# Kernel optimization log

Measured on AMD Instinct MI355X. Metric: run time of the kernel, lower is better.

The kernel has to match this reference:

```python
import jax, jax.numpy as jnp
import numpy as np

B, N, D = 64, 4096, 256      # batch, num_inputs, in_features
S, K, H = 11, 128, 256       # num_slots, slot_size, mlp_hidden_size
ITERS = 3
EPS = 1e-6
LN_EPS = 1e-5


def layer_norm(x, w, b):
    m = jnp.mean(x, axis=-1, keepdims=True)
    v = jnp.mean(jnp.square(x - m), axis=-1, keepdims=True)
    return (x - m) * jax.lax.rsqrt(v + LN_EPS) * w + b


def setup_inputs() -> dict:
    key = jax.random.key(0)
    ks = jax.random.split(key, 24)
    rn = lambda i, shape, sc=1.0: jax.random.normal(ks[i], shape, jnp.float32) * sc
    p = 0.05  # param init scale
    return {
        "inputs": rn(0, (B, N, D)),
        "slots_init": rn(1, (B, S, K)),
        "slots_mu": rn(2, (1, 1, K), p),
        "slots_log_sigma": rn(3, (1, 1, K), p),
        "ln_in_w": 1.0 + rn(4, (D,), p), "ln_in_b": rn(5, (D,), p),
        "ln_slot_w": 1.0 + rn(6, (K,), p), "ln_slot_b": rn(7, (K,), p),
        "ln_mlp_w": 1.0 + rn(8, (K,), p), "ln_mlp_b": rn(9, (K,), p),
        "Wq": rn(10, (K, K), p),
        "Wk": rn(11, (K, D), p),
        "Wv": rn(12, (K, D), p),
        "w_ih": rn(13, (3 * K, K), p), "w_hh": rn(14, (3 * K, K), p),
        "b_ih": rn(15, (3 * K,), p), "b_hh": rn(16, (3 * K,), p),
        "mlp_w1": rn(17, (H, K), p), "mlp_b1": rn(18, (H,), p),
        "mlp_w2": rn(19, (K, H), p), "mlp_b2": rn(20, (K,), p),
    }


def reference(inputs, slots_init, slots_mu, slots_log_sigma,
              ln_in_w, ln_in_b, ln_slot_w, ln_slot_b, ln_mlp_w, ln_mlp_b,
              Wq, Wk, Wv, w_ih, w_hh, b_ih, b_hh,
              mlp_w1, mlp_b1, mlp_w2, mlp_b2):
    x = layer_norm(inputs, ln_in_w, ln_in_b)            # [B,N,D]
    k = jnp.einsum('bnd,kd->bnk', x, Wk)                # [B,N,K]
    v = jnp.einsum('bnd,kd->bnk', x, Wv)                # [B,N,K]
    slots = slots_mu + jnp.exp(slots_log_sigma) * slots_init  # [B,S,K]
    scale = K ** -0.5
    for _ in range(ITERS):
        slots_prev = slots
        sn = layer_norm(slots, ln_slot_w, ln_slot_b)
        q = jnp.einsum('bsk,jk->bsj', sn, Wq)           # [B,S,K]
        logits = scale * jnp.einsum('bnk,bsk->bns', k, q)  # [B,N,S]
        attn = jax.nn.softmax(logits, axis=-1) + EPS    # softmax over slots
        attn = attn / jnp.sum(attn, axis=1, keepdims=True)  # renorm over inputs
        updates = jnp.einsum('bns,bnk->bsk', attn, v)   # [B,S,K]
        # GRUCell: input=updates, hidden=slots_prev
        gi = jnp.einsum('bsk,jk->bsj', updates, w_ih) + b_ih     # [B,S,3K]
        gh = jnp.einsum('bsk,jk->bsj', slots_prev, w_hh) + b_hh  # [B,S,3K]
        i_r, i_z, i_n = jnp.split(gi, 3, axis=-1)
        h_r, h_z, h_n = jnp.split(gh, 3, axis=-1)
        r = jax.nn.sigmoid(i_r + h_r)
        z = jax.nn.sigmoid(i_z + h_z)
        n = jnp.tanh(i_n + r * h_n)
        slots = (1.0 - z) * n + z * slots_prev
        m = layer_norm(slots, ln_mlp_w, ln_mlp_b)
        hid = jax.nn.relu(jnp.einsum('bsk,hk->bsh', m, mlp_w1) + mlp_b1)
        slots = slots + jnp.einsum('bsh,kh->bsk', hid, mlp_w2) + mlp_b2
    return slots
```

## Files before the change

### kernel.cpp

```cpp
#include <hip/hip_runtime.h>
#include <hip/hip_bf16.h>
#include <cstdint>
#include <cstddef>

#define B_ 64
#define N_ 4096
#define D_ 256
#define S_ 11
#define K_ 128
#define H_ 256
#define ITERS_ 3
#define EPS_ 1e-6f
#define LN_EPS_ 1e-5f
#define SCALE_ 0.08838834764831845f
#define NCH_ 16

typedef __bf16 bf16x8 __attribute__((ext_vector_type(8)));
typedef float  f32x4  __attribute__((ext_vector_type(4)));

__device__ __forceinline__ unsigned short f2bu(float f) {
  __bf16 h = (__bf16)f;
  return __builtin_bit_cast(unsigned short, h);
}
__device__ __forceinline__ unsigned int pk2(float a, float b) {
  return (unsigned int)f2bu(a) | ((unsigned int)f2bu(b) << 16);
}
__device__ __forceinline__ float b2f(unsigned int u16) {
  return __builtin_bit_cast(float, (u16 & 0xffffu) << 16);
}

__global__ __launch_bounds__(256) void kprep(const float* __restrict__ Wk,
                                             const float* __restrict__ Wv,
                                             const float* __restrict__ lnw,
                                             const float* __restrict__ lnb,
                                             unsigned short* __restrict__ W2pk,
                                             float* __restrict__ c1c2,
                                             const float* __restrict__ si,
                                             const float* __restrict__ mu,
                                             const float* __restrict__ ls,
                                             float* __restrict__ slots,
                                             const float* __restrict__ w_ih,
                                             const float* __restrict__ w_hh,
                                             unsigned int* __restrict__ wihP,
                                             unsigned int* __restrict__ whhP,
                                             const float* __restrict__ w1,
                                             unsigned int* __restrict__ w1P,
                                             const float* __restrict__ w2,
                                             unsigned int* __restrict__ w2P,
                                             const float* __restrict__ Wq,
                                             float* __restrict__ WqT,
                                             unsigned int* __restrict__ WqP) {
  int bid = blockIdx.x, t = threadIdx.x;
  if (bid < 32) {
    int f = bid * 256 + t;
    int ln_ = f & 63, jj = (f >> 6) & 3, kk2 = (f >> 8) & 1, kt = (f >> 9) & 3, ww = f >> 11;
    int row = ww * 64 + jj * 16 + (ln_ & 15);
    int col = kt * 64 + kk2 * 32 + (ln_ >> 4) * 8;
    const float* src = (row < 128) ? (Wk + row * 256 + col) : (Wv + (row - 128) * 256 + col);
    float4 a = *(const float4*)src;
    float4 b = *(const float4*)(src + 4);
    float4 l0 = *(const float4*)(lnw + col);
    float4 l1 = *(const float4*)(lnw + col + 4);
    a.x *= l0.x; a.y *= l0.y; a.z *= l0.z; a.w *= l0.w;
    b.x *= l1.x; b.y *= l1.y; b.z *= l1.z; b.w *= l1.w;
    uint4 u;
    u.x = pk2(a.x, a.y); u.y = pk2(a.z, a.w); u.z = pk2(b.x, b.y); u.w = pk2(b.z, b.w);
    *(uint4*)(W2pk + (size_t)f * 8) = u;
  } else if (bid < 384) {
    int i = (bid - 32) * 256 + t;
    int k = i & 127;
    slots[i] = mu[k] + __expf(ls[k]) * si[i];
  } else if (bid < 480) {
    int i = (bid - 384) * 256 + t;
    int kkp = i & 63, col = i >> 6;
    wihP[kkp * 384 + col] = pk2(w_ih[col * 128 + 2 * kkp], w_ih[col * 128 + 2 * kkp + 1]);
  } else if (bid < 576) {
    int i = (bid - 480) * 256 + t;
    int kkp = i & 63, col = i >> 6;
    whhP[kkp * 384 + col] = pk2(w_hh[col * 128 + 2 * kkp], w_hh[col * 128 + 2 * kkp + 1]);
  } else if (bid < 640) {
    int i = (bid - 576) * 256 + t;
    int kkp = i & 63, hc = i >> 6;
    w1P[kkp * 256 + hc] = pk2(w1[hc * 128 + 2 * kkp], w1[hc * 128 + 2 * kkp + 1]);
  } else if (bid < 704) {
    int i = (bid - 640) * 256 + t;
    int j = i & 127, hhp = i >> 7;
    w2P[hhp * 128 + j] = pk2(w2[j * 256 + 2 * hhp], w2[j * 256 + 2 * hhp + 1]);
  } else if (bid < 768) {
    int i = (bid - 704) * 256 + t;
    int r = i >> 7, c = i & 127;
    WqT[c * 128 + r] = Wq[i];
  } else if (bid < 800) {
    int i = (bid - 768) * 256 + t;
    int j = i & 127, mm = i >> 7;
    int kk0 = (mm >> 5) * 64 + (mm & 31) * 2;
    WqP[mm * 128 + j] = pk2(Wq[j * 128 + kk0], Wq[j * 128 + kk0 + 1]);
  } else {
    int j = t;
    const float* wrow = (j < 128) ? (Wk + j * 256) : (Wv + (j - 128) * 256);
    float c1 = 0.f, c2 = 0.f;
    for (int d = 0; d < 256; d++) {
      float wv = wrow[d];
      c1 += lnb[d] * wv;
      c2 += lnw[d] * wv;
    }
    c1c2[2 * j] = c1;
    c1c2[2 * j + 1] = c2;
  }
}

__global__ __launch_bounds__(256) void k12_lngemm(const float* __restrict__ x,
                                                  const float* __restrict__ c1c2,
                                                  const unsigned short* __restrict__ W2pk,
                                                  unsigned short* __restrict__ k_frag,
                                                  unsigned short* __restrict__ v_frag) {
  __shared__ char smem[32768];
  __shared__ float2 mu_a[64];
  __shared__ float2 ccs[256];
  const int t = threadIdx.x;
  const int lane = t & 63, w = t >> 6;
  const long rowg0 = (long)blockIdx.x * 64;

  ccs[t] = ((const float2*)c1c2)[t];

  bf16x8 bA[4], bB[4];
  auto loadB = [&](int kt, int kk, bf16x8* dst) {
#pragma unroll
    for (int jl = 0; jl < 4; jl++)
      dst[jl] = *(const bf16x8*)(W2pk +
          (size_t)((w << 11) | (kt << 9) | (kk << 8) | (jl << 6) | lane) * 8);
  };
  loadB(0, 0, bA);

  {
    const float* xb = x + (rowg0 + w * 16) * 256 + lane * 4;
#pragma unroll
    for (int rr = 0; rr < 16; rr++) {
      float4 xv = *(const float4*)(xb + rr * 256);
      int r = w * 16 + rr;
      uint2 pk;
      pk.x = pk2(xv.x, xv.y);
      pk.y = pk2(xv.z, xv.w);
      *(uint2*)(smem + r * 512 + (((lane >> 1) ^ (r & 7)) << 4) + ((lane & 1) << 3)) = pk;
    }
  }
  __syncthreads();

  {
    const int sr = t >> 2, squad = t & 3;
    float s = 0.f, ss = 0.f;
#pragma unroll
    for (int c8 = 0; c8 < 8; c8++) {
      bf16x8 v = *(const bf16x8*)(smem + sr * 512 + ((((squad * 8 + c8) ^ (sr & 7))) << 4));
#pragma unroll
      for (int e = 0; e < 8; e++) {
        float f = (float)v[e];
        s += f; ss += f * f;
      }
    }
    s += __shfl_xor(s, 1);  s += __shfl_xor(s, 2);
    ss += __shfl_xor(ss, 1); ss += __shfl_xor(ss, 2);
    if (squad == 0) {
      float m = s * (1.f / 256.f);
      float var = ss * (1.f / 256.f) - m * m;
      float2 ma; ma.x = m; ma.y = rsqrtf(var + LN_EPS_);
      mu_a[sr] = ma;
    }
  }

  f32x4 acc[4][4] = {};
#pragma unroll
  for (int sstep = 0; sstep < 8; sstep++) {
    const int kt = sstep >> 1, kk = sstep & 1;
    const bf16x8* cur = (sstep & 1) ? bB : bA;
    bf16x8* nxt = (sstep & 1) ? bA : bB;
    if (sstep < 7) loadB((sstep + 1) >> 1, (sstep + 1) & 1, nxt);
    bf16x8 xf[4];
#pragma unroll
    for (int i = 0; i < 4; i++) {
      int row = i * 16 + (lane & 15);
      int slot = (kt * 8 + kk * 4 + (lane >> 4)) ^ (lane & 7);
      xf[i] = *(const bf16x8*)(smem + row * 512 + (slot << 4));
    }
    if (w < 2) {
#pragma unroll
      for (int i = 0; i < 4; i++)
#pragma unroll
        for (int jl = 0; jl < 4; jl++)
          acc[i][jl] = __builtin_amdgcn_mfma_f32_16x16x32_bf16(cur[jl], xf[i], acc[i][jl], 0, 0, 0);
    } else {
#pragma unroll
      for (int i = 0; i < 4; i++)
#pragma unroll
        for (int jl = 0; jl < 4; jl++)
          acc[i][jl] = __builtin_amdgcn_mfma_f32_16x16x32_bf16(xf[i], cur[jl], acc[i][jl], 0, 0, 0);
    }
  }
  __syncthreads();

  const int ll = lane & 15, lh = lane >> 4;
  if (w < 2) {
    float2 ccr[4][4];
#pragma unroll
    for (int jl = 0; jl < 4; jl++) {
      int jg = w * 4 + jl;
#pragma unroll
      for (int reg = 0; reg < 4; reg++) ccr[jl][reg] = ccs[jg * 16 + lh * 4 + reg];
    }
#pragma unroll
    for (int i = 0; i < 4; i++) {
      float2 ma = mu_a[i * 16 + ll];
#pragma unroll
      for (int jl = 0; jl < 4; jl++) {
        int jg = w * 4 + jl;
        float v0 = ma.y * (acc[i][jl][0] - ma.x * ccr[jl][0].y) + ccr[jl][0].x;
        float v1 = ma.y * (acc[i][jl][1] - ma.x * ccr[jl][1].y) + ccr[jl][1].x;
        float v2 = ma.y * (acc[i][jl][2] - ma.x * ccr[jl][2].y) + ccr[jl][2].x;
        float v3 = ma.y * (acc[i][jl][3] - ma.x * ccr[jl][3].y) + ccr[jl][3].x;
        uint2 pk;
        pk.x = pk2(v0, v1); pk.y = pk2(v2, v3);
        size_t chunk = ((size_t)(rowg0 >> 4) + i) * 4 + (jg >> 1);
        int off = (ll + 16 * ((jg & 1) * 2 + (lh >> 1))) * 8 + (lh & 1) * 4;
        *(uint2*)(k_frag + chunk * 512 + off) = pk;
      }
    }
  } else {
    float2 cj[4];
#pragma unroll
    for (int jl = 0; jl < 4; jl++) cj[jl] = ccs[128 + (w - 2) * 64 + jl * 16 + ll];
#pragma unroll
    for (int i = 0; i < 4; i++) {
      float2 ma0 = mu_a[i * 16 + lh * 4 + 0];
      float2 ma1 = mu_a[i * 16 + lh * 4 + 1];
      float2 ma2 = mu_a[i * 16 + lh * 4 + 2];
      float2 ma3 = mu_a[i * 16 + lh * 4 + 3];
#pragma unroll
      for (int jl = 0; jl < 4; jl++) {
        float v0 = ma0.y * (acc[i][jl][0] - ma0.x * cj[jl].y) + cj[jl].x;
        float v1 = ma1.y * (acc[i][jl][1] - ma1.x * cj[jl].y) + cj[jl].x;
        float v2 = ma2.y * (acc[i][jl][2] - ma2.x * cj[jl].y) + cj[jl].x;
        float v3 = ma3.y * (acc[i][jl][3] - ma3.x * cj[jl].y) + cj[jl].x;
        uint2 pk;
        pk.x = pk2(v0, v1); pk.y = pk2(v2, v3);
        size_t chunk = ((size_t)(rowg0 >> 5) + (i >> 1)) * 8 + (w - 2) * 4 + jl;
        int off = (ll + 16 * ((i & 1) * 2 + (lh >> 1))) * 8 + (lh & 1) * 4;
        *(uint2*)(v_frag + chunk * 512 + off) = pk;
      }
    }
  }
}

__device__ __forceinline__ float redsum128(float v, float* red2) {
#pragma unroll
  for (int o = 1; o < 64; o <<= 1) v += __shfl_xor(v, o);
  __syncthreads();
  if ((threadIdx.x & 63) == 0) red2[threadIdx.x >> 6] = v;
  __syncthreads();
  return red2[0] + red2[1];
}

__global__ __launch_bounds__(128) void k3_q(const float* __restrict__ slots,
                                            const float* __restrict__ lw,
                                            const float* __restrict__ lb,
                                            const float* __restrict__ WqT,
                                            float* __restrict__ q) {
  int bs = blockIdx.x;
  int j = threadIdx.x;
  __shared__ float sn[128];
  __shared__ float red2[2];
  float x = slots[(size_t)bs * 128 + j];
  float sum = redsum128(x, red2);
  float sq  = redsum128(x * x, red2);
  float mean = sum * (1.f / 128.f);
  float var  = sq * (1.f / 128.f) - mean * mean;
  float v = (x - mean) * rsqrtf(var + LN_EPS_) * lw[j] + lb[j];
  sn[j] = v;
  __syncthreads();
  float acc = 0.f;
#pragma unroll 8
  for (int kk = 0; kk < 128; kk++) acc += sn[kk] * WqT[kk * 128 + j];
  q[(size_t)bs * 128 + j] = acc;
}

__global__ __launch_bounds__(256) void k45_attn(const unsigned short* __restrict__ k_frag,
                                                const unsigned short* __restrict__ v_frag,
                                                const float* __restrict__ qbuf,
                                                float* __restrict__ num_part,
                                                float* __restrict__ den_part) {
  __shared__ unsigned short att[16 * 264];
  __shared__ float redd[4][16];
  const int t = threadIdx.x;
  const int lane = t & 63, w = t >> 6;
  const int b = blockIdx.x >> 4, chunk = blockIdx.x & (NCH_ - 1);

  int sqi = lane & 15; if (sqi > 10) sqi = 10;
  const float* qp = qbuf + ((size_t)b * S_ + sqi) * 128 + (lane >> 4) * 8;
  bf16x8 qf[4];
#pragma unroll
  for (int ks = 0; ks < 4; ks++) {
    float4 q0 = *(const float4*)(qp + ks * 32);
    float4 q1 = *(const float4*)(qp + ks * 32 + 4);
    uint4 uu;
    uu.x = pk2(q0.x, q0.y); uu.y = pk2(q0.z, q0.w);
    uu.z = pk2(q1.x, q1.y); uu.w = pk2(q1.z, q1.w);
    qf[ks] = __builtin_bit_cast(bf16x8, uu);
  }
  const bool dead = (lane & 15) >= 11;
  float dden = 0.f;

#pragma unroll
  for (int u = 0; u < 4; u++) {
    size_t g = (size_t)b * 256 + chunk * 16 + w * 4 + u;
    f32x4 lg = {0.f, 0.f, 0.f, 0.f};
#pragma unroll
    for (int ks = 0; ks < 4; ks++) {
      bf16x8 af = *(const bf16x8*)(k_frag + (g * 4 + ks) * 512 + lane * 8);
      lg = __builtin_amdgcn_mfma_f32_16x16x32_bf16(af, qf[ks], lg, 0, 0, 0);
    }
    float l0 = dead ? -1e30f : lg[0] * SCALE_;
    float l1 = dead ? -1e30f : lg[1] * SCALE_;
    float l2 = dead ? -1e30f : lg[2] * SCALE_;
    float l3 = dead ? -1e30f : lg[3] * SCALE_;
    float m0 = l0, m1 = l1, m2 = l2, m3 = l3;
#pragma unroll
    for (int o = 1; o < 16; o <<= 1) {
      m0 = fmaxf(m0, __shfl_xor(m0, o)); m1 = fmaxf(m1, __shfl_xor(m1, o));
      m2 = fmaxf(m2, __shfl_xor(m2, o)); m3 = fmaxf(m3, __shfl_xor(m3, o));
    }
    float e0 = __expf(l0 - m0), e1 = __expf(l1 - m1);
    float e2 = __expf(l2 - m2), e3 = __expf(l3 - m3);
    float t0 = e0, t1 = e1, t2 = e2, t3 = e3;
#pragma unroll
    for (int o = 1; o < 16; o <<= 1) {
      t0 += __shfl_xor(t0, o); t1 += __shfl_xor(t1, o);
      t2 += __shfl_xor(t2, o); t3 += __shfl_xor(t3, o);
    }
    float a0 = e0 / t0 + EPS_, a1 = e1 / t1 + EPS_;
    float a2 = e2 / t2 + EPS_, a3 = e3 / t3 + EPS_;
    dden += a0 + a1 + a2 + a3;
    uint2 pk;
    pk.x = pk2(a0, a1); pk.y = pk2(a2, a3);
    int s = lane & 15;
    int nn = w * 64 + u * 16 + (lane >> 4) * 4;
    *(uint2*)((char*)att + s * 528 + nn * 2) = pk;
  }
  dden += __shfl_xor(dden, 16);
  dden += __shfl_xor(dden, 32);
  if (lane < 16) redd[w][lane] = dden;
  __syncthreads();
  if (t < S_)
    den_part[((size_t)b * NCH_ + chunk) * S_ + t] =
        redd[0][t] + redd[1][t] + redd[2][t] + redd[3][t];

  f32x4 acc[2] = {};
#pragma unroll
  for (int ks = 0; ks < 8; ks++) {
    bf16x8 pa = *(const bf16x8*)((const char*)att + (lane & 15) * 528 +
                                 (ks * 32 + (lane >> 4) * 8) * 2);
    size_t nb = (size_t)b * 128 + chunk * 8 + ks;
#pragma unroll
    for (int j = 0; j < 2; j++) {
      bf16x8 vb = *(const bf16x8*)(v_frag + (nb * 8 + (w * 2 + j)) * 512 + lane * 8);
      acc[j] = __builtin_amdgcn_mfma_f32_16x16x32_bf16(pa, vb, acc[j], 0, 0, 0);
    }
  }
#pragma unroll
  for (int j = 0; j < 2; j++)
#pragma unroll
    for (int r = 0; r < 4; r++) {
      int s = (lane >> 4) * 4 + r;
      if (s < S_) {
        int k = w * 32 + j * 16 + (lane & 15);
        num_part[(((size_t)b * NCH_ + chunk) * S_ + s) * 128 + k] = acc[j][r];
      }
    }
}

__global__ __launch_bounds__(256) void k63_final(const float* __restrict__ num_part,
                                                 const float* __restrict__ den_part,
                                                 float* __restrict__ slots,
                                                 const unsigned int* __restrict__ wihP,
                                                 const unsigned int* __restrict__ whhP,
                                                 const float* __restrict__ b_ih,
                                                 const float* __restrict__ b_hh,
                                                 const float* __restrict__ lmw,
                                                 const float* __restrict__ lmb,
                                                 const unsigned int* __restrict__ w1P,
                                                 const float* __restrict__ bb1,
                                                 const unsigned int* __restrict__ w2P,
                                                 const float* __restrict__ bb2,
                                                 const float* __restrict__ lsw,
                                                 const float* __restrict__ lsb,
                                                 const unsigned int* __restrict__ WqP,
                                                 float* __restrict__ qbuf,
                                                 float* __restrict__ outp,
                                                 int cq, int wout) {
  int bs = blockIdx.x;
  int b = bs / S_, s = bs % S_;
  int t = threadIdx.x;
  int j = t & 127, half = t >> 7;
  __shared__ float u[128], h[128], gp[3][128], m[128], hid[256], sjs[128], op[128];
  __shared__ float ns[128], snq[128];
  __shared__ float red2a[2], red2b[2];

  if (half == 0) {
    float den = 0.f;
#pragma unroll
    for (int c = 0; c < NCH_; c++) den += den_part[((size_t)b * NCH_ + c) * S_ + s];
    float uj = 0.f;
#pragma unroll
    for (int c = 0; c < NCH_; c++) uj += num_part[(((size_t)b * NCH_ + c) * S_ + s) * 128 + j];
    u[j] = uj / den;
  } else {
    h[j] = slots[((size_t)b * S_ + s) * 128 + j];
  }
  __syncthreads();

  {
    const unsigned int* wP = half ? whhP : wihP;
    const float* sv = half ? h : u;
    float g0 = 0.f, g1 = 0.f, g2 = 0.f;
#pragma unroll 8
    for (int kkp = 0; kkp < 64; kkp++) {
      float s0 = sv[2 * kkp], s1 = sv[2 * kkp + 1];
      unsigned int a0 = wP[kkp * 384 + j];
      unsigned int a1 = wP[kkp * 384 + 128 + j];
      unsigned int a2 = wP[kkp * 384 + 256 + j];
      g0 += b2f(a0) * s0 + b2f(a0 >> 16) * s1;
      g1 += b2f(a1) * s0 + b2f(a1 >> 16) * s1;
      g2 += b2f(a2) * s0 + b2f(a2 >> 16) * s1;
    }
    if (half) { gp[0][j] = g0; gp[1][j] = g1; gp[2][j] = g2; }
    __syncthreads();
    float sj = 0.f;
    if (half == 0) {
      float gr = g0 + b_ih[j]       + gp[0][j] + b_hh[j];
      float gz = g1 + b_ih[128 + j] + gp[1][j] + b_hh[128 + j];
      float r = 1.f / (1.f + __expf(-gr));
      float z = 1.f / (1.f + __expf(-gz));
      float nn = tanhf(g2 + b_ih[256 + j] + r * (gp[2][j] + b_hh[256 + j]));
      sj = (1.f - z) * nn + z * h[j];
      sjs[j] = sj;
    }
    float sv2 = sj, sq2 = sj * sj;
#pragma unroll
    for (int o = 1; o < 64; o <<= 1) { sv2 += __shfl_xor(sv2, o); sq2 += __shfl_xor(sq2, o); }
    if (half == 0 && (t & 63) == 0) { red2a[t >> 6] = sv2; red2b[t >> 6] = sq2; }
    __syncthreads();
    float mean = (red2a[0] + red2a[1]) * (1.f / 128.f);
    float var  = (red2b[0] + red2b[1]) * (1.f / 128.f) - mean * mean;
    float rstd = rsqrtf(var + LN_EPS_);
    if (half == 0) m[j] = (sj - mean) * rstd * lmw[j] + lmb[j];
  }
  __syncthreads();

  {
    float a = bb1[t];
#pragma unroll 8
    for (int kkp = 0; kkp < 64; kkp++) {
      unsigned int wv = w1P[kkp * 256 + t];
      a += b2f(wv) * m[2 * kkp] + b2f(wv >> 16) * m[2 * kkp + 1];
    }
    hid[t] = fmaxf(a, 0.f);
  }
  __syncthreads();

  {
    const float* hp = hid + half * 128;
    float o2 = 0.f;
#pragma unroll 8
    for (int hhp = 0; hhp < 64; hhp++) {
      unsigned int wv = w2P[(half * 64 + hhp) * 128 + j];
      o2 += b2f(wv) * hp[2 * hhp] + b2f(wv >> 16) * hp[2 * hhp + 1];
    }
    if (half) op[j] = o2;
    __syncthreads();
    if (half == 0) {
      float ov = sjs[j] + bb2[j] + o2 + op[j];
      slots[((size_t)b * S_ + s) * 128 + j] = ov;
      if (wout) outp[((size_t)b * S_ + s) * 128 + j] = ov;
      ns[j] = ov;
    }
  }
  __syncthreads();

  if (cq) {
    float vv = (half == 0) ? ns[j] : 0.f;
    float s1 = vv, s2 = vv * vv;
#pragma unroll
    for (int o = 1; o < 64; o <<= 1) { s1 += __shfl_xor(s1, o); s2 += __shfl_xor(s2, o); }
    if (half == 0 && (t & 63) == 0) { red2a[t >> 6] = s1; red2b[t >> 6] = s2; }
    __syncthreads();
    float mean = (red2a[0] + red2a[1]) * (1.f / 128.f);
    float var  = (red2b[0] + red2b[1]) * (1.f / 128.f) - mean * mean;
    float rstd = rsqrtf(var + LN_EPS_);
    if (half == 0) snq[j] = (ns[j] - mean) * rstd * lsw[j] + lsb[j];
    __syncthreads();
    const float* sp = snq + half * 64;
    float qv = 0.f;
#pragma unroll 8
    for (int m2 = 0; m2 < 32; m2++) {
      unsigned int wv = WqP[(half * 32 + m2) * 128 + j];
      qv += b2f(wv) * sp[2 * m2] + b2f(wv >> 16) * sp[2 * m2 + 1];
    }
    if (half) op[j] = qv;
    __syncthreads();
    if (half == 0) qbuf[(size_t)bs * 128 + j] = qv + op[j];
  }
}

extern "C" void kernel_launch(void* const* d_in, const int* in_sizes, int n_in,
                              void* d_out, int out_size, void* d_ws, size_t ws_size,
                              hipStream_t stream) {
  (void)in_sizes; (void)n_in; (void)out_size; (void)ws_size;
  const float* inputs     = (const float*)d_in[0];
  const float* slots_init = (const float*)d_in[1];
  const float* slots_mu   = (const float*)d_in[2];
  const float* slots_ls   = (const float*)d_in[3];
  const float* ln_in_w    = (const float*)d_in[4];
  const float* ln_in_b    = (const float*)d_in[5];
  const float* ln_slot_w  = (const float*)d_in[6];
  const float* ln_slot_b  = (const float*)d_in[7];
  const float* ln_mlp_w   = (const float*)d_in[8];
  const float* ln_mlp_b   = (const float*)d_in[9];
  const float* Wq         = (const float*)d_in[10];
  const float* Wk         = (const float*)d_in[11];
  const float* Wv         = (const float*)d_in[12];
  const float* w_ih       = (const float*)d_in[13];
  const float* w_hh       = (const float*)d_in[14];
  const float* b_ih       = (const float*)d_in[15];
  const float* b_hh       = (const float*)d_in[16];
  const float* mlp_w1     = (const float*)d_in[17];
  const float* mlp_b1     = (const float*)d_in[18];
  const float* mlp_w2     = (const float*)d_in[19];
  const float* mlp_b2     = (const float*)d_in[20];

  uintptr_t p = (uintptr_t)d_ws;
  auto carve = [&](size_t bytes) -> void* {
    void* r = (void*)p;
    p += (bytes + 255) & ~(size_t)255;
    return r;
  };
  unsigned short* k_frag = (unsigned short*)carve((size_t)B_ * N_ * K_ * 2);
  unsigned short* v_frag = (unsigned short*)carve((size_t)B_ * K_ * N_ * 2);
  unsigned short* W2pk   = (unsigned short*)carve((size_t)256 * 256 * 2);
  float* c1c2  = (float*)carve((size_t)256 * 2 * 4);
  unsigned int* wihP = (unsigned int*)carve((size_t)64 * 384 * 4);
  unsigned int* whhP = (unsigned int*)carve((size_t)64 * 384 * 4);
  unsigned int* w1P  = (unsigned int*)carve((size_t)64 * 256 * 4);
  unsigned int* w2P  = (unsigned int*)carve((size_t)128 * 128 * 4);
  unsigned int* WqP  = (unsigned int*)carve((size_t)64 * 128 * 4);
  float* WqT   = (float*)carve((size_t)128 * 128 * 4);
  float* qbuf     = (float*)carve((size_t)B_ * S_ * K_ * 4);
  float* slots    = (float*)carve((size_t)B_ * S_ * K_ * 4);
  float* den_part = (float*)carve((size_t)B_ * NCH_ * S_ * 4);
  float* num_part = (float*)carve((size_t)B_ * NCH_ * S_ * K_ * 4);

  kprep<<<801, 256, 0, stream>>>(Wk, Wv, ln_in_w, ln_in_b, W2pk, c1c2,
                                 slots_init, slots_mu, slots_ls, slots,
                                 w_ih, w_hh, wihP, whhP, mlp_w1, w1P, mlp_w2, w2P,
                                 Wq, WqT, WqP);
  k12_lngemm<<<(B_ * N_) / 64, 256, 0, stream>>>(inputs, c1c2, W2pk, k_frag, v_frag);
  k3_q<<<B_ * S_, 128, 0, stream>>>(slots, ln_slot_w, ln_slot_b, WqT, qbuf);

  for (int it = 0; it < ITERS_; ++it) {
    k45_attn<<<B_ * NCH_, 256, 0, stream>>>(k_frag, v_frag, qbuf, num_part, den_part);
    k63_final<<<B_ * S_, 256, 0, stream>>>(num_part, den_part, slots,
                                           wihP, whhP, b_ih, b_hh,
                                           ln_mlp_w, ln_mlp_b,
                                           w1P, mlp_b1, w2P, mlp_b2,
                                           ln_slot_w, ln_slot_b, WqP, qbuf,
                                           (float*)d_out,
                                           (it < ITERS_ - 1) ? 1 : 0,
                                           (it == ITERS_ - 1) ? 1 : 0);
  }
}
```

Before: 232.5 us.

## Warp-specialize LN-GEMM into persistent producer/consumer pipeline over tiles

```diff
diff --git a/kernel.cpp b/kernel.cpp
--- a/kernel.cpp
+++ b/kernel.cpp
@@ -14,6 +14,7 @@
 #define LN_EPS_ 1e-5f
 #define SCALE_ 0.08838834764831845f
 #define NCH_ 16
+#define TPB_ 16
 
 typedef __bf16 bf16x8 __attribute__((ext_vector_type(8)));
 typedef float  f32x4  __attribute__((ext_vector_type(4)));
@@ -109,143 +110,150 @@
   }
 }
 
-__global__ __launch_bounds__(256) void k12_lngemm(const float* __restrict__ x,
+__global__ __launch_bounds__(512) void k12_lngemm(const float* __restrict__ x,
                                                   const float* __restrict__ c1c2,
                                                   const unsigned short* __restrict__ W2pk,
                                                   unsigned short* __restrict__ k_frag,
                                                   unsigned short* __restrict__ v_frag) {
-  __shared__ char smem[32768];
-  __shared__ float2 mu_a[64];
+  __shared__ char smem[2][32768];
+  __shared__ float2 mu_a[2][64];
   __shared__ float2 ccs[256];
   const int t = threadIdx.x;
   const int lane = t & 63, w = t >> 6;
-  const long rowg0 = (long)blockIdx.x * 64;
-
-  ccs[t] = ((const float2*)c1c2)[t];
-
-  bf16x8 bA[4], bB[4];
-  auto loadB = [&](int kt, int kk, bf16x8* dst) {
-#pragma unroll
-    for (int jl = 0; jl < 4; jl++)
-      dst[jl] = *(const bf16x8*)(W2pk +
-          (size_t)((w << 11) | (kt << 9) | (kk << 8) | (jl << 6) | lane) * 8);
-  };
-  loadB(0, 0, bA);
-
-  {
-    const float* xb = x + (rowg0 + w * 16) * 256 + lane * 4;
-#pragma unroll
-    for (int rr = 0; rr < 16; rr++) {
-      float4 xv = *(const float4*)(xb + rr * 256);
-      int r = w * 16 + rr;
-      uint2 pk;
-      pk.x = pk2(xv.x, xv.y);
-      pk.y = pk2(xv.z, xv.w);
-      *(uint2*)(smem + r * 512 + (((lane >> 1) ^ (r & 7)) << 4) + ((lane & 1) << 3)) = pk;
-    }
-  }
-  __syncthreads();
-
-  {
-    const int sr = t >> 2, squad = t & 3;
-    float s = 0.f, ss = 0.f;
-#pragma unroll
-    for (int c8 = 0; c8 < 8; c8++) {
-      bf16x8 v = *(const bf16x8*)(smem + sr * 512 + ((((squad * 8 + c8) ^ (sr & 7))) << 4));
-#pragma unroll
-      for (int e = 0; e < 8; e++) {
-        float f = (float)v[e];
-        s += f; ss += f * f;
+  const long tile0 = (long)blockIdx.x * TPB_;
+
+  if (t < 256) ccs[t] = ((const float2*)c1c2)[t];
+
+  if (w < 4) {
+    for (int tt = 0; tt < TPB_ + 1; tt++) {
+      if (tt < TPB_) {
+        char* buf = smem[tt & 1];
+        const float* xb = x + ((tile0 + tt) * 64 + w * 16) * 256 + lane * 4;
+#pragma unroll
+        for (int h8 = 0; h8 < 2; h8++) {
+          float4 xa[8];
+#pragma unroll
+          for (int rr = 0; rr < 8; rr++) xa[rr] = *(const float4*)(xb + (h8 * 8 + rr) * 256);
+#pragma unroll
+          for (int rr = 0; rr < 8; rr++) {
+            float4 xv = xa[rr];
+            int r = w * 16 + h8 * 8 + rr;
+            uint2 pk;
+            pk.x = pk2(xv.x, xv.y);
+            pk.y = pk2(xv.z, xv.w);
+            *(uint2*)(buf + r * 512 + (((lane >> 1) ^ (r & 7)) << 4) + ((lane & 1) << 3)) = pk;
+            float s  = xv.x + xv.y + xv.z + xv.w;
+            float ss = xv.x * xv.x + xv.y * xv.y + xv.z * xv.z + xv.w * xv.w;
+#pragma unroll
+            for (int o = 1; o < 64; o <<= 1) { s += __shfl_xor(s, o); ss += __shfl_xor(ss, o); }
+            if (lane == 0) {
+              float m = s * (1.f / 256.f);
+              float var = ss * (1.f / 256.f) - m * m;
+              float2 ma; ma.x = m; ma.y = rsqrtf(var + LN_EPS_);
+              mu_a[tt & 1][r] = ma;
+            }
+          }
+        }
       }
-    }
-    s += __shfl_xor(s, 1);  s += __shfl_xor(s, 2);
-    ss += __shfl_xor(ss, 1); ss += __shfl_xor(ss, 2);
-    if (squad == 0) {
-      float m = s * (1.f / 256.f);
-      float var = ss * (1.f / 256.f) - m * m;
-      float2 ma; ma.x = m; ma.y = rsqrtf(var + LN_EPS_);
-      mu_a[sr] = ma;
-    }
-  }
-
-  f32x4 acc[4][4] = {};
-#pragma unroll
-  for (int sstep = 0; sstep < 8; sstep++) {
-    const int kt = sstep >> 1, kk = sstep & 1;
-    const bf16x8* cur = (sstep & 1) ? bB : bA;
-    bf16x8* nxt = (sstep & 1) ? bA : bB;
-    if (sstep < 7) loadB((sstep + 1) >> 1, (sstep + 1) & 1, nxt);
-    bf16x8 xf[4];
-#pragma unroll
-    for (int i = 0; i < 4; i++) {
-      int row = i * 16 + (lane & 15);
-      int slot = (kt * 8 + kk * 4 + (lane >> 4)) ^ (lane & 7);
-      xf[i] = *(const bf16x8*)(smem + row * 512 + (slot << 4));
-    }
-    if (w < 2) {
-#pragma unroll
-      for (int i = 0; i < 4; i++)
-#pragma unroll
-        for (int jl = 0; jl < 4; jl++)
-          acc[i][jl] = __builtin_amdgcn_mfma_f32_16x16x32_bf16(cur[jl], xf[i], acc[i][jl], 0, 0, 0);
-    } else {
-#pragma unroll
-      for (int i = 0; i < 4; i++)
-#pragma unroll
-        for (int jl = 0; jl < 4; jl++)
-          acc[i][jl] = __builtin_amdgcn_mfma_f32_16x16x32_bf16(xf[i], cur[jl], acc[i][jl], 0, 0, 0);
-    }
-  }
-  __syncthreads();
-
-  const int ll = lane & 15, lh = lane >> 4;
-  if (w < 2) {
-    float2 ccr[4][4];
-#pragma unroll
-    for (int jl = 0; jl < 4; jl++) {
-      int jg = w * 4 + jl;
-#pragma unroll
-      for (int reg = 0; reg < 4; reg++) ccr[jl][reg] = ccs[jg * 16 + lh * 4 + reg];
-    }
-#pragma unroll
-    for (int i = 0; i < 4; i++) {
-      float2 ma = mu_a[i * 16 + ll];
-#pragma unroll
-      for (int jl = 0; jl < 4; jl++) {
-        int jg = w * 4 + jl;
-        float v0 = ma.y * (acc[i][jl][0] - ma.x * ccr[jl][0].y) + ccr[jl][0].x;
-        float v1 = ma.y * (acc[i][jl][1] - ma.x * ccr[jl][1].y) + ccr[jl][1].x;
-        float v2 = ma.y * (acc[i][jl][2] - ma.x * ccr[jl][2].y) + ccr[jl][2].x;
-        float v3 = ma.y * (acc[i][jl][3] - ma.x * ccr[jl][3].y) + ccr[jl][3].x;
-        uint2 pk;
-        pk.x = pk2(v0, v1); pk.y = pk2(v2, v3);
-        size_t chunk = ((size_t)(rowg0 >> 4) + i) * 4 + (jg >> 1);
-        int off = (ll + 16 * ((jg & 1) * 2 + (lh >> 1))) * 8 + (lh & 1) * 4;
-        *(uint2*)(k_frag + chunk * 512 + off) = pk;
+      __syncthreads();
+    }
+  } else {
+    const int cw = w - 4;
+    const int ll = lane & 15, lh = lane >> 4;
+    bf16x8 bA[4], bB[4];
+    auto loadB = [&](int kt, int kk, bf16x8* dst) {
+#pragma unroll
+      for (int jl = 0; jl < 4; jl++)
+        dst[jl] = *(const bf16x8*)(W2pk +
+            (size_t)((cw << 11) | (kt << 9) | (kk << 8) | (jl << 6) | lane) * 8);
+    };
+    loadB(0, 0, bA);
+    for (int tt = 0; tt < TPB_ + 1; tt++) {
+      if (tt >= 1) {
+        const int p = (tt - 1) & 1;
+        const char* buf = smem[p];
+        const long rowg0 = (tile0 + tt - 1) * 64;
+        f32x4 acc[4][4] = {};
+#pragma unroll
+        for (int sstep = 0; sstep < 8; sstep++) {
+          const int kt = sstep >> 1, kk = sstep & 1;
+          const bf16x8* cur = (sstep & 1) ? bB : bA;
+          bf16x8* nxt = (sstep & 1) ? bA : bB;
+          if (sstep < 7) loadB((sstep + 1) >> 1, (sstep + 1) & 1, nxt);
+          bf16x8 xf[4];
+#pragma unroll
+          for (int i = 0; i < 4; i++) {
+            int row = i * 16 + ll;
+            int slot = (kt * 8 + kk * 4 + lh) ^ (lane & 7);
+            xf[i] = *(const bf16x8*)(buf + row * 512 + (slot << 4));
+          }
+          if (cw < 2) {
+#pragma unroll
+            for (int i = 0; i < 4; i++)
+#pragma unroll
+              for (int jl = 0; jl < 4; jl++)
+                acc[i][jl] = __builtin_amdgcn_mfma_f32_16x16x32_bf16(cur[jl], xf[i], acc[i][jl], 0, 0, 0);
+          } else {
+#pragma unroll
+            for (int i = 0; i < 4; i++)
+#pragma unroll
+              for (int jl = 0; jl < 4; jl++)
+                acc[i][jl] = __builtin_amdgcn_mfma_f32_16x16x32_bf16(xf[i], cur[jl], acc[i][jl], 0, 0, 0);
+          }
+        }
+        loadB(0, 0, bA);
+
+        if (cw < 2) {
+          float2 ccr[4][4];
+#pragma unroll
+          for (int jl = 0; jl < 4; jl++) {
+            int jg = cw * 4 + jl;
+#pragma unroll
+            for (int reg = 0; reg < 4; reg++) ccr[jl][reg] = ccs[jg * 16 + lh * 4 + reg];
+          }
+#pragma unroll
+          for (int i = 0; i < 4; i++) {
+            float2 ma = mu_a[p][i * 16 + ll];
+#pragma unroll
+            for (int jl = 0; jl < 4; jl++) {
+              int jg = cw * 4 + jl;
+              float v0 = ma.y * (acc[i][jl][0] - ma.x * ccr[jl][0].y) + ccr[jl][0].x;
+              float v1 = ma.y * (acc[i][jl][1] - ma.x * ccr[jl][1].y) + ccr[jl][1].x;
+              float v2 = ma.y * (acc[i][jl][2] - ma.x * ccr[jl][2].y) + ccr[jl][2].x;
+              float v3 = ma.y * (acc[i][jl][3] - ma.x * ccr[jl][3].y) + ccr[jl][3].x;
+              uint2 pk;
+              pk.x = pk2(v0, v1); pk.y = pk2(v2, v3);
+              size_t chunk = ((size_t)(rowg0 >> 4) + i) * 4 + (jg >> 1);
+              int off = (ll + 16 * ((jg & 1) * 2 + (lh >> 1))) * 8 + (lh & 1) * 4;
+              *(uint2*)(k_frag + chunk * 512 + off) = pk;
+            }
+          }
+        } else {
+          float2 cj[4];
+#pragma unroll
+          for (int jl = 0; jl < 4; jl++) cj[jl] = ccs[128 + (cw - 2) * 64 + jl * 16 + ll];
+#pragma unroll
+          for (int i = 0; i < 4; i++) {
+            float2 ma0 = mu_a[p][i * 16 + lh * 4 + 0];
+            float2 ma1 = mu_a[p][i * 16 + lh * 4 + 1];
+            float2 ma2 = mu_a[p][i * 16 + lh * 4 + 2];
+            float2 ma3 = mu_a[p][i * 16 + lh * 4 + 3];
+#pragma unroll
+            for (int jl = 0; jl < 4; jl++) {
+              float v0 = ma0.y * (acc[i][jl][0] - ma0.x * cj[jl].y) + cj[jl].x;
+              float v1 = ma1.y * (acc[i][jl][1] - ma1.x * cj[jl].y) + cj[jl].x;
+              float v2 = ma2.y * (acc[i][jl][2] - ma2.x * cj[jl].y) + cj[jl].x;
+              float v3 = ma3.y * (acc[i][jl][3] - ma3.x * cj[jl].y) + cj[jl].x;
+              uint2 pk;
+              pk.x = pk2(v0, v1); pk.y = pk2(v2, v3);
+              size_t chunk = ((size_t)(rowg0 >> 5) + (i >> 1)) * 8 + (cw - 2) * 4 + jl;
+              int off = (ll + 16 * ((i & 1) * 2 + (lh >> 1))) * 8 + (lh & 1) * 4;
+              *(uint2*)(v_frag + chunk * 512 + off) = pk;
+            }
+          }
+        }
       }
-    }
-  } else {
-    float2 cj[4];
-#pragma unroll
-    for (int jl = 0; jl < 4; jl++) cj[jl] = ccs[128 + (w - 2) * 64 + jl * 16 + ll];
-#pragma unroll
-    for (int i = 0; i < 4; i++) {
-      float2 ma0 = mu_a[i * 16 + lh * 4 + 0];
-      float2 ma1 = mu_a[i * 16 + lh * 4 + 1];
-      float2 ma2 = mu_a[i * 16 + lh * 4 + 2];
-      float2 ma3 = mu_a[i * 16 + lh * 4 + 3];
-#pragma unroll
-      for (int jl = 0; jl < 4; jl++) {
-        float v0 = ma0.y * (acc[i][jl][0] - ma0.x * cj[jl].y) + cj[jl].x;
-        float v1 = ma1.y * (acc[i][jl][1] - ma1.x * cj[jl].y) + cj[jl].x;
-        float v2 = ma2.y * (acc[i][jl][2] - ma2.x * cj[jl].y) + cj[jl].x;
-        float v3 = ma3.y * (acc[i][jl][3] - ma3.x * cj[jl].y) + cj[jl].x;
-        uint2 pk;
-        pk.x = pk2(v0, v1); pk.y = pk2(v2, v3);
-        size_t chunk = ((size_t)(rowg0 >> 5) + (i >> 1)) * 8 + (w - 2) * 4 + jl;
-        int off = (ll + 16 * ((i & 1) * 2 + (lh >> 1))) * 8 + (lh & 1) * 4;
-        *(uint2*)(v_frag + chunk * 512 + off) = pk;
-      }
+      __syncthreads();
     }
   }
 }
@@ -560,7 +568,7 @@
                                  slots_init, slots_mu, slots_ls, slots,
                                  w_ih, w_hh, wihP, whhP, mlp_w1, w1P, mlp_w2, w2P,
                                  Wq, WqT, WqP);
-  k12_lngemm<<<(B_ * N_) / 64, 256, 0, stream>>>(inputs, c1c2, W2pk, k_frag, v_frag);
+  k12_lngemm<<<(B_ * N_) / (64 * TPB_), 512, 0, stream>>>(inputs, c1c2, W2pk, k_frag, v_frag);
   k3_q<<<B_ * S_, 128, 0, stream>>>(slots, ln_slot_w, ln_slot_b, WqT, qbuf);
 
   for (int it = 0; it < ITERS_; ++it) {
```

Result: slower. 265.0 us (+14.0%).
